# Performance work log

Measured on AMD Instinct MI355X. Metric: run time of the kernel, lower is better.

Reference implementation:

```python
import jax, jax.numpy as jnp
import numpy as np

NUM_HEADS = 16
NUM_GROUPS = 4
HIDDEN = 2048
HEAD_DIM = HIDDEN // NUM_HEADS  # 128


def setup_inputs() -> dict:
    key = jax.random.key(0)
    ks = jax.random.split(key, 9)
    B, S = 2, 2048
    kv_dim = NUM_GROUPS * HEAD_DIM
    sc_in = 1.0 / np.sqrt(HIDDEN)
    return {
        "X": jax.random.normal(ks[0], (B, S, HIDDEN), dtype=jnp.float32),
        "Wq": jax.random.normal(ks[1], (HIDDEN, HIDDEN), dtype=jnp.float32) * sc_in,
        "bq": jnp.zeros((HIDDEN,), jnp.float32),
        "Wk": jax.random.normal(ks[2], (kv_dim, HIDDEN), dtype=jnp.float32) * sc_in,
        "bk": jnp.zeros((kv_dim,), jnp.float32),
        "Wv": jax.random.normal(ks[3], (kv_dim, HIDDEN), dtype=jnp.float32) * sc_in,
        "bv": jnp.zeros((kv_dim,), jnp.float32),
        "Wo": jax.random.normal(ks[4], (HIDDEN, HIDDEN), dtype=jnp.float32) * sc_in,
        "bo": jnp.zeros((HIDDEN,), jnp.float32),
    }


def reference(X, Wq, bq, Wk, bk, Wv, bv, Wo, bo):
    B, S, D = X.shape
    H, G, hd = NUM_HEADS, NUM_GROUPS, HEAD_DIM
    rep = H // G

    q = X @ Wq.T + bq                          # (B,S,D)
    k = X @ Wk.T + bk                          # (B,S,G*hd)
    v = X @ Wv.T + bv                          # (B,S,G*hd)

    q = q.reshape(B, S, H, hd).transpose(0, 2, 1, 3)   # (B,H,S,hd)
    k = k.reshape(B, S, G, hd).transpose(0, 2, 1, 3)   # (B,G,S,hd)
    v = v.reshape(B, S, G, hd).transpose(0, 2, 1, 3)
    # GQA head expansion: each kv group serves rep query heads
    k = jnp.repeat(k, rep, axis=1)             # (B,H,S,hd)
    v = jnp.repeat(v, rep, axis=1)

    scale = 1.0 / jnp.sqrt(jnp.asarray(hd, X.dtype))
    scores = jnp.einsum('bhqd,bhkd->bhqk', q, k) * scale  # (B,H,S,S)
    attn = jax.nn.softmax(scores, axis=-1)
    mid = jnp.einsum('bhqk,bhkd->bhqd', attn, v)          # (B,H,S,hd)
    mid = mid.transpose(0, 2, 1, 3).reshape(B, S, D)
    return mid @ Wo.T + bo
```

## Files before the change

kernel.cpp:

```cpp
#include <hip/hip_runtime.h>

using uint = unsigned int;
using ushort = unsigned short;

typedef float f32x4 __attribute__((ext_vector_type(4)));
typedef float f32x16 __attribute__((ext_vector_type(16)));
typedef uint u32x4 __attribute__((ext_vector_type(4)));
using short8 = __attribute__((ext_vector_type(8))) short;

__device__ __forceinline__ ushort f2bf(float f) {
  uint u = __float_as_uint(f);
  u += 0x7fffu + ((u >> 16) & 1u);
  return (ushort)(u >> 16);
}

#define GLOAD_LDS16(gptr, lptr)                                                   \
  __builtin_amdgcn_global_load_lds(                                               \
      (const __attribute__((address_space(1))) void*)(gptr),                      \
      (__attribute__((address_space(3))) void*)(lptr), 16, 0, 0)

__global__ void cast_all_bf16(const float* __restrict__ X,
                              const float* __restrict__ Wq,
                              const float* __restrict__ Wk,
                              const float* __restrict__ Wv,
                              const float* __restrict__ Wo,
                              ushort* __restrict__ dst ) {
  const int e0 = 2097152;
  const int e1 = e0 + 1048576;
  const int e2 = e1 + 262144;
  const int e3 = e2 + 262144;
  const int e4 = e3 + 1048576;
  const int stride = gridDim.x * blockDim.x;
  for (int i = blockIdx.x * blockDim.x + threadIdx.x; i < e4; i += stride) {
    const float* src;
    int j;
    if (i < e0)      { src = X;  j = i; }
    else if (i < e1) { src = Wq; j = i - e0; }
    else if (i < e2) { src = Wk; j = i - e1; }
    else if (i < e3) { src = Wv; j = i - e2; }
    else             { src = Wo; j = i - e3; }
    float4 v = reinterpret_cast<const float4*>(src)[j];
    ushort4 o;
    o.x = f2bf(v.x); o.y = f2bf(v.y); o.z = f2bf(v.z); o.w = f2bf(v.w);
    reinterpret_cast<ushort4*>(dst)[i] = o;
  }
}

__device__ __forceinline__ void gemm128_mainloop(const ushort* __restrict__ A,
                                                 const ushort* __restrict__ W,
                                                 int K, ushort* As, ushort* Bs,
                                                 f32x4 (&acc)[4][4]) {
  const int tid = threadIdx.x;
  const int lane = tid & 63;
  const int wr = (tid >> 7) & 1;
  const int wc = (tid >> 6) & 1;
  const char* aP = (const char*)(A + (size_t)(tid >> 2) * K) + (tid & 3) * 16;
  const char* bP = (const char*)(W + (size_t)(tid >> 2) * K) + (tid & 3) * 16;
  const size_t rowHop = (size_t)64 * K * 2;
  ushort* aL0 = As + tid * 8;
  ushort* aL1 = As + 2048 + tid * 8;
  ushort* bL0 = Bs + tid * 8;
  ushort* bL1 = Bs + 2048 + tid * 8;
  const int ar = lane & 15;
  const int ak = (lane >> 4) * 8;

  for (int k0 = 0; k0 < K; k0 += 32) {
    GLOAD_LDS16(aP, aL0);
    GLOAD_LDS16(aP + rowHop, aL1);
    GLOAD_LDS16(bP, bL0);
    GLOAD_LDS16(bP + rowHop, bL1);
    aP += 64; bP += 64;
    __syncthreads();
    short8 af[4], bf[4];
#pragma unroll
    for (int i = 0; i < 4; ++i)
      af[i] = *reinterpret_cast<const short8*>(&As[(wr * 64 + i * 16 + ar) * 32 + ak]);
#pragma unroll
    for (int i = 0; i < 4; ++i)
      bf[i] = *reinterpret_cast<const short8*>(&Bs[(wc * 64 + i * 16 + ar) * 32 + ak]);
#pragma unroll
    for (int mi = 0; mi < 4; ++mi)
#pragma unroll
      for (int ni = 0; ni < 4; ++ni)
        acc[mi][ni] = __builtin_amdgcn_mfma_f32_16x16x32_bf16(af[mi], bf[ni],
                                                              acc[mi][ni], 0, 0, 0);
    __syncthreads();
  }
}

__global__ __launch_bounds__(256) void qkv_gemm(
    const ushort* __restrict__ Xb, const ushort* __restrict__ Wq,
    const ushort* __restrict__ Wk, const ushort* __restrict__ Wv,
    const float* __restrict__ bq, const float* __restrict__ bk,
    const float* __restrict__ bv, ushort* __restrict__ Qb,
    ushort* __restrict__ Kb, ushort* __restrict__ Vt) {
  __shared__ ushort As[128 * 32], Bs[128 * 32];
  const int bx = blockIdx.x, by = blockIdx.y;
  const ushort* W; const float* bias; ushort* out;
  int n0, mode, ldo;
  if (bx < 16)      { W = Wq; bias = bq; out = Qb; n0 = bx * 128;        mode = 0; ldo = 2048; }
  else if (bx < 20) { W = Wk; bias = bk; out = Kb; n0 = (bx - 16) * 128; mode = 0; ldo = 512; }
  else              { W = Wv; bias = bv; out = Vt; n0 = (bx - 20) * 128; mode = 1; ldo = 0; }

  f32x4 acc[4][4] = {};
  gemm128_mainloop(Xb + (size_t)by * 128 * 2048, W + (size_t)n0 * 2048, 2048, As, Bs, acc);

  const int lane = threadIdx.x & 63;
  const int wr = (threadIdx.x >> 7) & 1, wc = (threadIdx.x >> 6) & 1;
  const int r0 = by * 128 + wr * 64 + ((lane >> 4) * 4);
  const int c0 = wc * 64 + (lane & 15);
#pragma unroll
  for (int mi = 0; mi < 4; ++mi)
#pragma unroll
    for (int ni = 0; ni < 4; ++ni) {
      const int col = c0 + ni * 16;
      const float bb = bias[n0 + col];
#pragma unroll
      for (int j = 0; j < 4; ++j) {
        const int row = r0 + mi * 16 + j;
        const float v = acc[mi][ni][j] + bb;
        if (mode == 0) {
          out[(size_t)row * ldo + n0 + col] = f2bf(v);
        } else {
          const int b = row >> 11, s = row & 2047;
          out[((size_t)(b * 512 + n0 + col) << 11) + s] = f2bf(v);
        }
      }
    }
}

__global__ __launch_bounds__(256) void out_gemm(const ushort* __restrict__ Mid,
                                                const ushort* __restrict__ Wo,
                                                const float* __restrict__ bo,
                                                float* __restrict__ Out) {
  __shared__ ushort As[128 * 32], Bs[128 * 32];
  const int bx = blockIdx.x, by = blockIdx.y;
  f32x4 acc[4][4] = {};
  gemm128_mainloop(Mid + (size_t)by * 128 * 2048, Wo + (size_t)bx * 128 * 2048,
                   2048, As, Bs, acc);
  const int lane = threadIdx.x & 63;
  const int wr = (threadIdx.x >> 7) & 1, wc = (threadIdx.x >> 6) & 1;
  const int r0 = by * 128 + wr * 64 + ((lane >> 4) * 4);
  const int c0 = bx * 128 + wc * 64 + (lane & 15);
#pragma unroll
  for (int mi = 0; mi < 4; ++mi)
#pragma unroll
    for (int ni = 0; ni < 4; ++ni) {
      const int col = c0 + ni * 16;
      const float bb = bo[col];
#pragma unroll
      for (int j = 0; j < 4; ++j)
        Out[(size_t)(r0 + mi * 16 + j) * 2048 + col] = acc[mi][ni][j] + bb;
    }
}

__global__ __launch_bounds__(256, 2) void attn_fwd(const ushort* __restrict__ Q,
                                                   const ushort* __restrict__ Kb,
                                                   const ushort* __restrict__ Vt,
                                                   ushort* __restrict__ Mid) {
  __shared__ ushort Ks[2][64 * 128];
  __shared__ ushort Vs[2][128 * 64];

  const int tid = threadIdx.x, lane = tid & 63, wave = tid >> 6;
  const int h = blockIdx.y, b = blockIdx.z, g = h >> 2;
  const int q0w = blockIdx.x * 128 + wave * 32;
  const int lq = lane & 31, hi = lane >> 5;

  const char* kbase = (const char*)Kb + ((size_t)b * 2048 * 512 + g * 128) * 2;
  const char* vbase = (const char*)Vt + ((size_t)(b * 512 + g * 128) * 2048) * 2;
  int kRow[4], kOff[4], vRow[4], vOff[4];
#pragma unroll
  for (int i = 0; i < 4; ++i) {
    const int off = (i * 256 + tid) * 16;
    const int r = off >> 8, c = off & 255;
    kRow[i] = r; kOff[i] = c ^ ((r & 15) << 4);
    const int rv = off >> 7, cv = off & 127;
    vRow[i] = rv; vOff[i] = cv ^ ((rv & 7) << 4);
  }

#pragma unroll
  for (int i = 0; i < 4; ++i) {
    GLOAD_LDS16(kbase + (size_t)kRow[i] * 1024 + kOff[i],
                (char*)Ks[0] + (i * 256 + tid) * 16);
    GLOAD_LDS16(vbase + (size_t)vRow[i] * 4096 + vOff[i],
                (char*)Vs[0] + (i * 256 + tid) * 16);
  }

  short8 qf[8];
  {
    const ushort* qp = Q + (size_t)(b * 2048 + q0w + lq) * 2048 + h * 128 + hi * 8;
#pragma unroll
    for (int dblk = 0; dblk < 8; ++dblk)
      qf[dblk] = *reinterpret_cast<const short8*>(qp + dblk * 16);
  }

  float m_s = -3.0e38f, l_s = 0.f;
  f32x16 o[4] = {};
  const float sc2 = 0.08838834764831843f * 1.44269504088896340736f;

  __syncthreads();

  const int ksw = (lq & 15) << 4;

  for (int t = 0; t < 32; ++t) {
    const int cur = t & 1;
    if (t < 31) {
      const int kv0 = (t + 1) * 64;
#pragma unroll
      for (int i = 0; i < 4; ++i) {
        GLOAD_LDS16(kbase + (size_t)(kv0 + kRow[i]) * 1024 + kOff[i],
                    (char*)Ks[cur ^ 1] + (i * 256 + tid) * 16);
        GLOAD_LDS16(vbase + (size_t)vRow[i] * 4096 + kv0 * 2 + vOff[i],
                    (char*)Vs[cur ^ 1] + (i * 256 + tid) * 16);
      }
    }

    const char* ksb = (const char*)Ks[cur];
    f32x16 st0 = {}, st1 = {};
    __builtin_amdgcn_s_setprio(1);
#pragma unroll
    for (int dblk = 0; dblk < 8; ++dblk) {
      const int cb = (dblk * 32 + 16 * hi) ^ ksw;
      short8 kf0 = *reinterpret_cast<const short8*>(ksb + lq * 256 + cb);
      short8 kf1 = *reinterpret_cast<const short8*>(ksb + (32 + lq) * 256 + cb);
      st0 = __builtin_amdgcn_mfma_f32_32x32x16_bf16(kf0, qf[dblk], st0, 0, 0, 0);
      st1 = __builtin_amdgcn_mfma_f32_32x32x16_bf16(kf1, qf[dblk], st1, 0, 0, 0);
    }
    __builtin_amdgcn_s_setprio(0);

    float mx[16];
#pragma unroll
    for (int r = 0; r < 16; ++r) mx[r] = fmaxf(st0[r], st1[r]);
#pragma unroll
    for (int s = 8; s >= 1; s >>= 1)
#pragma unroll
      for (int r = 0; r < s; ++r) mx[r] = fmaxf(mx[r], mx[r + s]);
    float pm = fmaxf(mx[0], __shfl_xor(mx[0], 32, 64));
    const float msc = pm * sc2;

    if (__any(msc > m_s + 8.f)) {
      const float mnew = fmaxf(m_s, msc);
      const float alpha = exp2f(m_s - mnew);
      m_s = mnew;
      l_s *= alpha;
#pragma unroll
      for (int r = 0; r < 16; ++r) {
        const int qr = (r & 3) + 8 * (r >> 2) + 4 * hi;
        const float ar = __shfl(alpha, qr, 64);
#pragma unroll
        for (int dblk = 0; dblk < 4; ++dblk) o[dblk][r] *= ar;
      }
    }

    float sm[16];
#pragma unroll
    for (int r = 0; r < 16; ++r) {
      st0[r] = exp2f(fmaf(st0[r], sc2, -m_s));
      st1[r] = exp2f(fmaf(st1[r], sc2, -m_s));
      sm[r] = st0[r] + st1[r];
    }
#pragma unroll
    for (int s = 8; s >= 1; s >>= 1)
#pragma unroll
      for (int r = 0; r < s; ++r) sm[r] += sm[r + s];
    float rs = sm[0];
    rs += __shfl_xor(rs, 32, 64);
    l_s += rs;

    short8 pa[4];
#pragma unroll
    for (int half = 0; half < 2; ++half) {
      const f32x16 pt = half ? st1 : st0;
#pragma unroll
      for (int kk = 0; kk < 2; ++kk) {
        const int Rx = kk * 8;
        uint w0, w1, w2, w3;
#pragma unroll
        for (int s2 = 0; s2 < 2; ++s2) {
          const int s = s2 * 2;
          const float x0 = pt[Rx + s],     x1 = pt[Rx + s + 1];
          const float y0 = pt[Rx + 4 + s], y1 = pt[Rx + 4 + s + 1];
          uint x, y;
          asm("v_cvt_pk_bf16_f32 %0, %1, %2" : "=v"(x) : "v"(x0), "v"(x1));
          asm("v_cvt_pk_bf16_f32 %0, %1, %2" : "=v"(y) : "v"(y0), "v"(y1));
          auto sw = __builtin_amdgcn_permlane32_swap(x, y, false, false);
          if (s2 == 0) { w0 = sw[0]; w2 = sw[1]; }
          else         { w1 = sw[0]; w3 = sw[1]; }
        }
        u32x4 wv = {w0, w1, w2, w3};
        pa[half * 2 + kk] = __builtin_bit_cast(short8, wv);
      }
    }

    const char* vsb = (const char*)Vs[cur];
    __builtin_amdgcn_s_setprio(1);
#pragma unroll
    for (int dblk = 0; dblk < 4; ++dblk) {
      const int rv = dblk * 32 + lq;
      const int vsw2 = (rv & 7) << 4;
#pragma unroll
      for (int ks = 0; ks < 4; ++ks) {
        short8 vf = *reinterpret_cast<const short8*>(
            vsb + rv * 128 + ((ks * 32 + 16 * hi) ^ vsw2));
        o[dblk] = __builtin_amdgcn_mfma_f32_32x32x16_bf16(pa[ks], vf, o[dblk], 0, 0, 0);
      }
    }
    __builtin_amdgcn_s_setprio(0);

    __syncthreads();
  }

  const float linv = 1.f / l_s;
#pragma unroll
  for (int r = 0; r < 16; ++r) {
    const int qr = (r & 3) + 8 * (r >> 2) + 4 * hi;
    const float lv = __shfl(linv, qr, 64);
    ushort* mp = Mid + (size_t)(b * 2048 + q0w + qr) * 2048 + h * 128 + lq;
#pragma unroll
    for (int dblk = 0; dblk < 4; ++dblk)
      mp[dblk * 32] = f2bf(o[dblk][r] * lv);
  }
}

extern "C" void kernel_launch(void* const* d_in, const int* in_sizes, int n_in,
                              void* d_out, int out_size, void* d_ws, size_t ws_size,
                              hipStream_t stream) {
  const float* X  = (const float*)d_in[0];
  const float* Wq = (const float*)d_in[1];
  const float* bq = (const float*)d_in[2];
  const float* Wk = (const float*)d_in[3];
  const float* bk = (const float*)d_in[4];
  const float* Wv = (const float*)d_in[5];
  const float* bv = (const float*)d_in[6];
  const float* Wo = (const float*)d_in[7];
  const float* bo = (const float*)d_in[8];
  float* Out = (float*)d_out;

  char* ws = (char*)d_ws;
  ushort* Xb   = (ushort*)(ws);
  ushort* Wqb  = (ushort*)(ws + 16777216);
  ushort* Wkb  = (ushort*)(ws + 25165824);
  ushort* Wvb  = (ushort*)(ws + 27262976);
  ushort* Wob  = (ushort*)(ws + 29360128);
  ushort* Qb   = (ushort*)(ws + 37748736);
  ushort* Kbuf = (ushort*)(ws + 54525952);
  ushort* Vtb  = (ushort*)(ws + 58720256);
  ushort* Midb = (ushort*)(ws + 62914560);

  cast_all_bf16<<<dim3(2048), dim3(256), 0, stream>>>(X, Wq, Wk, Wv, Wo, Xb);

  qkv_gemm<<<dim3(24, 32), 256, 0, stream>>>(Xb, Wqb, Wkb, Wvb, bq, bk, bv,
                                             Qb, Kbuf, Vtb);
  attn_fwd<<<dim3(16, 16, 2), 256, 0, stream>>>(Qb, Kbuf, Vtb, Midb);
  out_gemm<<<dim3(16, 32), 256, 0, stream>>>(Midb, Wob, bo, Out);
}
```

Before: 224.9 us.

## Store V pre-swizzled in MFMA fragment order and load directly to registers

The QKV GEMM now writes V in a layout that matches the per-lane B-fragment order of the PV MFMA. The attention kernel then loads each 64-key V tile straight from global memory into registers, with no LDS staging. This frees half of the shared memory and removes the V LDS reads and writes, but the global loads for each tile are issued in the same iteration they are used and are no longer prefetched. It also replaces the cross-half shuffle reductions with permlane32_swap.

```diff
diff --git a/kernel.cpp b/kernel.cpp
--- a/kernel.cpp
+++ b/kernel.cpp
@@ -12,6 +12,13 @@
   uint u = __float_as_uint(f);
   u += 0x7fffu + ((u >> 16) & 1u);
   return (ushort)(u >> 16);
+}
+
+__device__ __forceinline__ void xhalf(float v, float& a, float& b) {
+  auto sw = __builtin_amdgcn_permlane32_swap(__float_as_uint(v), __float_as_uint(v),
+                                             false, false);
+  a = __uint_as_float(sw[0]);
+  b = __uint_as_float(sw[1]);
 }
 
 #define GLOAD_LDS16(gptr, lptr)                                                   \
@@ -93,14 +100,14 @@
     const ushort* __restrict__ Wk, const ushort* __restrict__ Wv,
     const float* __restrict__ bq, const float* __restrict__ bk,
     const float* __restrict__ bv, ushort* __restrict__ Qb,
-    ushort* __restrict__ Kb, ushort* __restrict__ Vt) {
+    ushort* __restrict__ Kb, ushort* __restrict__ Vf) {
   __shared__ ushort As[128 * 32], Bs[128 * 32];
   const int bx = blockIdx.x, by = blockIdx.y;
   const ushort* W; const float* bias; ushort* out;
   int n0, mode, ldo;
   if (bx < 16)      { W = Wq; bias = bq; out = Qb; n0 = bx * 128;        mode = 0; ldo = 2048; }
   else if (bx < 20) { W = Wk; bias = bk; out = Kb; n0 = (bx - 16) * 128; mode = 0; ldo = 512; }
-  else              { W = Wv; bias = bv; out = Vt; n0 = (bx - 20) * 128; mode = 1; ldo = 0; }
+  else              { W = Wv; bias = bv; out = Vf; n0 = (bx - 20) * 128; mode = 1; ldo = 0; }
 
   f32x4 acc[4][4] = {};
   gemm128_mainloop(Xb + (size_t)by * 128 * 2048, W + (size_t)n0 * 2048, 2048, As, Bs, acc);
@@ -122,8 +129,13 @@
         if (mode == 0) {
           out[(size_t)row * ldo + n0 + col] = f2bf(v);
         } else {
-          const int b = row >> 11, s = row & 2047;
-          out[((size_t)(b * 512 + n0 + col) << 11) + s] = f2bf(v);
+          const int b2 = row >> 11, s = row & 2047;
+          const int vc = n0 + col;
+          const int g2 = vc >> 7, d = vc & 127;
+          const int t2 = s >> 6, ks = (s >> 4) & 3, hi2 = (s >> 3) & 1, j2 = s & 7;
+          const int dblk = d >> 5, lq2 = d & 31;
+          out[(size_t)((b2 * 4 + g2) * 32 + t2) * 8192 +
+              (ks * 4 + dblk) * 512 + (hi2 * 32 + lq2) * 8 + j2] = f2bf(v);
         }
       }
     }
@@ -156,10 +168,9 @@
 
 __global__ __launch_bounds__(256, 2) void attn_fwd(const ushort* __restrict__ Q,
                                                    const ushort* __restrict__ Kb,
-                                                   const ushort* __restrict__ Vt,
+                                                   const ushort* __restrict__ Vf,
                                                    ushort* __restrict__ Mid) {
   __shared__ ushort Ks[2][64 * 128];
-  __shared__ ushort Vs[2][128 * 64];
 
   const int tid = threadIdx.x, lane = tid & 63, wave = tid >> 6;
   const int h = blockIdx.y, b = blockIdx.z, g = h >> 2;
@@ -167,24 +178,20 @@
   const int lq = lane & 31, hi = lane >> 5;
 
   const char* kbase = (const char*)Kb + ((size_t)b * 2048 * 512 + g * 128) * 2;
-  const char* vbase = (const char*)Vt + ((size_t)(b * 512 + g * 128) * 2048) * 2;
-  int kRow[4], kOff[4], vRow[4], vOff[4];
+  int kRow[4], kOff[4];
 #pragma unroll
   for (int i = 0; i < 4; ++i) {
     const int off = (i * 256 + tid) * 16;
     const int r = off >> 8, c = off & 255;
     kRow[i] = r; kOff[i] = c ^ ((r & 15) << 4);
-    const int rv = off >> 7, cv = off & 127;
-    vRow[i] = rv; vOff[i] = cv ^ ((rv & 7) << 4);
-  }
-
-#pragma unroll
-  for (int i = 0; i < 4; ++i) {
+  }
+
+#pragma unroll
+  for (int i = 0; i < 4; ++i)
     GLOAD_LDS16(kbase + (size_t)kRow[i] * 1024 + kOff[i],
                 (char*)Ks[0] + (i * 256 + tid) * 16);
-    GLOAD_LDS16(vbase + (size_t)vRow[i] * 4096 + vOff[i],
-                (char*)Vs[0] + (i * 256 + tid) * 16);
-  }
+
+  const ushort* vfb = Vf + (size_t)(b * 4 + g) * 262144 + lane * 8;
 
   short8 qf[8];
   {
@@ -204,15 +211,21 @@
 
   for (int t = 0; t < 32; ++t) {
     const int cur = t & 1;
+
+    short8 vr[16];
+    {
+      const ushort* vt = vfb + t * 8192;
+#pragma unroll
+      for (int u = 0; u < 16; ++u)
+        vr[u] = *reinterpret_cast<const short8*>(vt + u * 512);
+    }
+
     if (t < 31) {
       const int kv0 = (t + 1) * 64;
 #pragma unroll
-      for (int i = 0; i < 4; ++i) {
+      for (int i = 0; i < 4; ++i)
         GLOAD_LDS16(kbase + (size_t)(kv0 + kRow[i]) * 1024 + kOff[i],
                     (char*)Ks[cur ^ 1] + (i * 256 + tid) * 16);
-        GLOAD_LDS16(vbase + (size_t)vRow[i] * 4096 + kv0 * 2 + vOff[i],
-                    (char*)Vs[cur ^ 1] + (i * 256 + tid) * 16);
-      }
     }
 
     const char* ksb = (const char*)Ks[cur];
@@ -235,8 +248,9 @@
     for (int s = 8; s >= 1; s >>= 1)
 #pragma unroll
       for (int r = 0; r < s; ++r) mx[r] = fmaxf(mx[r], mx[r + s]);
-    float pm = fmaxf(mx[0], __shfl_xor(mx[0], 32, 64));
-    const float msc = pm * sc2;
+    float xa, xb;
+    xhalf(mx[0], xa, xb);
+    const float msc = fmaxf(xa, xb) * sc2;
 
     if (__any(msc > m_s + 8.f)) {
       const float mnew = fmaxf(m_s, msc);
@@ -263,9 +277,9 @@
     for (int s = 8; s >= 1; s >>= 1)
 #pragma unroll
       for (int r = 0; r < s; ++r) sm[r] += sm[r + s];
-    float rs = sm[0];
-    rs += __shfl_xor(rs, 32, 64);
-    l_s += rs;
+    float sa, sb;
+    xhalf(sm[0], sa, sb);
+    l_s += sa + sb;
 
     short8 pa[4];
 #pragma unroll
@@ -292,19 +306,13 @@
       }
     }
 
-    const char* vsb = (const char*)Vs[cur];
     __builtin_amdgcn_s_setprio(1);
 #pragma unroll
-    for (int dblk = 0; dblk < 4; ++dblk) {
-      const int rv = dblk * 32 + lq;
-      const int vsw2 = (rv & 7) << 4;
-#pragma unroll
-      for (int ks = 0; ks < 4; ++ks) {
-        short8 vf = *reinterpret_cast<const short8*>(
-            vsb + rv * 128 + ((ks * 32 + 16 * hi) ^ vsw2));
-        o[dblk] = __builtin_amdgcn_mfma_f32_32x32x16_bf16(pa[ks], vf, o[dblk], 0, 0, 0);
-      }
-    }
+    for (int dblk = 0; dblk < 4; ++dblk)
+#pragma unroll
+      for (int ks = 0; ks < 4; ++ks)
+        o[dblk] = __builtin_amdgcn_mfma_f32_32x32x16_bf16(pa[ks], vr[ks * 4 + dblk],
+                                                          o[dblk], 0, 0, 0);
     __builtin_amdgcn_s_setprio(0);
 
     __syncthreads();
@@ -344,13 +352,13 @@
   ushort* Wob  = (ushort*)(ws + 29360128);
   ushort* Qb   = (ushort*)(ws + 37748736);
   ushort* Kbuf = (ushort*)(ws + 54525952);
-  ushort* Vtb  = (ushort*)(ws + 58720256);
+  ushort* Vfb  = (ushort*)(ws + 58720256);
   ushort* Midb = (ushort*)(ws + 62914560);
 
   cast_all_bf16<<<dim3(2048), dim3(256), 0, stream>>>(X, Wq, Wk, Wv, Wo, Xb);
 
   qkv_gemm<<<dim3(24, 32), 256, 0, stream>>>(Xb, Wqb, Wkb, Wvb, bq, bk, bv,
-                                             Qb, Kbuf, Vtb);
-  attn_fwd<<<dim3(16, 16, 2), 256, 0, stream>>>(Qb, Kbuf, Vtb, Midb);
+                                             Qb, Kbuf, Vfb);
+  attn_fwd<<<dim3(16, 16, 2), 256, 0, stream>>>(Qb, Kbuf, Vfb, Midb);
   out_gemm<<<dim3(16, 32), 256, 0, stream>>>(Midb, Wob, bo, Out);
 }
```

Result: no change. 221.4 us (-1.5%).
